# Optimization experiments

Hardware: AMD Instinct MI355X
Metric: run time of the kernel (lower is better)

The kernel has to match this reference:

```python
import jax, jax.numpy as jnp
import numpy as np


def _diag_perm(h, w):
    # Matches torch loop: offsets -(h-1)..w-1, within offset ordered by row i.
    ii, jj = np.meshgrid(np.arange(h), np.arange(w), indexing='ij')
    idx = np.lexsort((ii.ravel(), (jj - ii).ravel())).astype(np.int32)
    inv = np.argsort(idx).astype(np.int32)
    return jnp.asarray(idx), jnp.asarray(inv)


def _mamba(tok, ln_g, ln_b, Win, conv_w, conv_b, Wx, Wdt, bdt, A_log, Dp, Wout):
    # tok: (B, L, C). MambaLayer = LayerNorm + standard Mamba block.
    di, dc = conv_w.shape
    ds = A_log.shape[-1]
    dtr = Wdt.shape[-1]
    mu = tok.mean(-1, keepdims=True)
    var = ((tok - mu) ** 2).mean(-1, keepdims=True)
    t = (tok - mu) * jax.lax.rsqrt(var + 1e-5) * ln_g + ln_b
    xz = jnp.einsum('blc,ec->ble', t, Win)          # (B,L,2*di)
    xh, z = jnp.split(xz, 2, axis=-1)
    # causal depthwise conv over sequence
    xc = jnp.transpose(xh, (0, 2, 1))               # (B,di,L)
    xc = jax.lax.conv_general_dilated(
        xc, conv_w[:, None, :], (1,), [(dc - 1, 0)],
        dimension_numbers=('NCH', 'OIH', 'NCH'), feature_group_count=di)
    u = jax.nn.silu(jnp.transpose(xc, (0, 2, 1)) + conv_b)  # (B,L,di)
    proj = jnp.einsum('bld,ed->ble', u, Wx)
    dt_r, Bm, Cm = jnp.split(proj, [dtr, dtr + ds], axis=-1)
    dt = jax.nn.softplus(jnp.einsum('blr,dr->bld', dt_r, Wdt) + bdt)  # (B,L,di)
    A = -jnp.exp(A_log)                              # (di,ds)

    def step(h, inp):
        dt_t, B_t, C_t, u_t = inp                    # (B,di) (B,ds) (B,ds) (B,di)
        dA = jnp.exp(dt_t[..., None] * A)            # (B,di,ds)
        h = dA * h + dt_t[..., None] * B_t[:, None, :] * u_t[..., None]
        y = jnp.einsum('bds,bs->bd', h, C_t)
        return h, y

    h0 = jnp.zeros((u.shape[0], di, ds), u.dtype)
    _, ys = jax.lax.scan(step, h0, (jnp.moveaxis(dt, 1, 0), jnp.moveaxis(Bm, 1, 0),
                                    jnp.moveaxis(Cm, 1, 0), jnp.moveaxis(u, 1, 0)))
    y = jnp.moveaxis(ys, 0, 1) + u * Dp              # (B,L,di)
    y = y * jax.nn.silu(z)
    return jnp.einsum('bld,cd->blc', y, Wout)


def _forward(x, ln_g, ln_b, Win, conv_w, conv_b, Wx, Wdt, bdt, A_log, Dp, Wout):
    b, c, h, w = x.shape
    idx, inv = _diag_perm(h, w)

    def mam(d, tok):
        return _mamba(tok, ln_g[d], ln_b[d], Win[d], conv_w[d], conv_b[d],
                      Wx[d], Wdt[d], bdt[d], A_log[d], Dp[d], Wout[d])

    row_tok = x.reshape(b, c, h * w).transpose(0, 2, 1)
    row_feat = mam(0, row_tok).transpose(0, 2, 1).reshape(b, c, h, w)
    col_tok = x.transpose(0, 1, 3, 2).reshape(b, c, w * h).transpose(0, 2, 1)
    col_feat = mam(1, col_tok).transpose(0, 2, 1).reshape(b, c, w, h).transpose(0, 1, 3, 2)
    diag_feat = mam(2, row_tok[:, idx, :])[:, inv, :].transpose(0, 2, 1).reshape(b, c, h, w)
    xf = x[:, :, :, ::-1]
    anti_tok = xf.reshape(b, c, h * w).transpose(0, 2, 1)[:, idx, :]
    anti_feat = mam(3, anti_tok)[:, inv, :].transpose(0, 2, 1).reshape(b, c, h, w)[:, :, :, ::-1]
    gate = jax.nn.sigmoid((row_feat + col_feat + diag_feat + anti_feat) / 4.0)
    return x * gate


def setup_inputs() -> dict:
    key = jax.random.key(0)
    ks = jax.random.split(key, 8)
    B, C, H, W = 4, 96, 48, 48
    DI, DS, DC, DTR = 192, 16, 4, 6
    s = 0.05
    return {
        'x': jax.random.normal(ks[0], (B, C, H, W), jnp.float32),
        'ln_g': jnp.ones((4, C), jnp.float32),
        'ln_b': jnp.zeros((4, C), jnp.float32),
        'Win': jax.random.normal(ks[1], (4, 2 * DI, C), jnp.float32) * s,
        'conv_w': jax.random.normal(ks[2], (4, DI, DC), jnp.float32) * s,
        'conv_b': jnp.zeros((4, DI), jnp.float32),
        'Wx': jax.random.normal(ks[3], (4, DTR + 2 * DS, DI), jnp.float32) * s,
        'Wdt': jax.random.normal(ks[4], (4, DI, DTR), jnp.float32) * s,
        'bdt': jax.random.normal(ks[5], (4, DI), jnp.float32) * s,
        'A_log': jnp.log(jnp.broadcast_to(jnp.arange(1, DS + 1, dtype=jnp.float32), (4, DI, DS))),
        'Dp': jnp.ones((4, DI), jnp.float32),
        'Wout': jax.random.normal(ks[6], (4, C, DI), jnp.float32) * s,
    }


def reference(x, ln_g, ln_b, Win, conv_w, conv_b, Wx, Wdt, bdt, A_log, Dp, Wout):
    return _forward(x, ln_g, ln_b, Win, conv_w, conv_b, Wx, Wdt, bdt, A_log, Dp, Wout)
```

## Files before the change

### kernel.cpp

```cpp
#include <hip/hip_runtime.h>
#include <math.h>

#define LSEQ 2304
#define LC 32
#define NCH 72

typedef unsigned short u16;
typedef unsigned int u32;
typedef __attribute__((ext_vector_type(8))) short bf16x8;
typedef __attribute__((ext_vector_type(4))) float f32x4;

__device__ __forceinline__ float sigmoidf_(float v){ return 1.f/(1.f+__expf(-v)); }
__device__ __forceinline__ u16 f2b(float f){
  union{float f; u32 u;} v; v.f = f;
  u32 r = v.u + 0x7fffu + ((v.u >> 16) & 1u);
  return (u16)(r >> 16);
}
__device__ __forceinline__ float b2f(u16 h){
  union{u32 u; float f;} v; v.u = ((u32)h) << 16; return v.f;
}
__device__ __forceinline__ u16 f2h(float f){
  _Float16 h = (_Float16)f;
  union{_Float16 h; u16 u;} v; v.h = h; return v.u;
}
__device__ __forceinline__ float h2f(u16 u){
  union{u16 u; _Float16 h;} v; v.u = u; return (float)v.h;
}
__device__ __forceinline__ uint2 pack4(float a, float b, float c, float d){
  uint2 o;
  o.x = (u32)f2b(a) | ((u32)f2b(b) << 16);
  o.y = (u32)f2b(c) | ((u32)f2b(d) << 16);
  return o;
}
__device__ __forceinline__ float softplus_(float v){
  return fmaxf(v, 0.f) + __logf(1.f + __expf(-fabsf(v)));
}

__global__ void g_kernel(int* __restrict__ g, int* __restrict__ flag){
  int tid = threadIdx.x;
  if (tid == 0) *flag = 1;
  for (int l = tid; l < LSEQ; l += 256){
    g[l] = l;
    g[LSEQ + l] = (l % 48) * 48 + l / 48;
  }
  for (int p = tid; p < LSEQ; p += 256){
    int i = p / 48, j = p % 48, dd = j - i;
    int off = (dd <= 0) ? (47 + dd) * (48 + dd) / 2
                        : 1176 + 48 * (dd - 1) - dd * (dd - 1) / 2;
    int l = off + min(i, j);
    g[2 * LSEQ + l] = p;
  }
  __syncthreads();
  for (int l = tid; l < LSEQ; l += 256){
    int p2 = g[2 * LSEQ + l];
    g[3 * LSEQ + l] = (p2 / 48) * 48 + 47 - (p2 % 48);
  }
}

__global__ void prep_fold(const float* __restrict__ Win, const float* __restrict__ ln_g,
                          const float* __restrict__ ln_b, const float* __restrict__ A_log,
                          const float* __restrict__ Wout, const float* __restrict__ Wx,
                          const float* __restrict__ Wdt, const float* __restrict__ bdt,
                          u16* __restrict__ WinMF, float* __restrict__ b2,
                          float* __restrict__ Aneg2, u16* __restrict__ WoutMF,
                          u16* __restrict__ Wcomb, float* __restrict__ bcomb,
                          int* __restrict__ flag){
  int i = blockIdx.x * 256 + threadIdx.x;
  if (i < 4*192*16){
    float a = -expf(A_log[i]);
    Aneg2[i] = a * 1.44269504f;
    int s = i & 15;
    float a0 = -expf(A_log[i - s]);
    if (fabsf(a - (float)(s + 1) * a0) > 1e-5f * fabsf(a) + 1e-30f)
      atomicAnd(flag, 0);
  }
  if (i < 4*384*96){
    int d = i / 36864, r = i % 36864, c = r % 96;
    WinMF[i] = f2b(Win[i] * ln_g[d*96 + c]);
  }
  if (i < 4*96*192) WoutMF[i] = f2b(Wout[i]);
  if (i < 4*224*192){
    int d = i / 43008, r = i % 43008, e = r / 192, c = r % 192;
    float w;
    if (e < 192){
      const float* wdt = &Wdt[(size_t)(d*192 + e) * 6];
      w = 0.f;
      #pragma unroll
      for (int r6 = 0; r6 < 6; ++r6) w += wdt[r6] * Wx[(size_t)(d*38 + r6) * 192 + c];
    } else if (e < 208){
      w = Wx[(size_t)(d*38 + 6 + (e - 192)) * 192 + c];
    } else {
      w = Wx[(size_t)(d*38 + 22 + (e - 208)) * 192 + c];
    }
    Wcomb[i] = f2b(w);
  }
  if (i < 4*224){
    int d = i / 224, e = i % 224;
    bcomb[i] = (e < 192) ? bdt[d*192 + e] : 0.f;
  }
  if (i < 4*384){
    int d = i / 384;
    const float* wr = &Win[(size_t)i * 96];
    const float* lb = &ln_b[d * 96];
    float s = 0.f;
    for (int c = 0; c < 96; ++c) s += wr[c] * lb[c];
    b2[i] = s;
  }
}

__global__ __launch_bounds__(256) void ln_kernel(const float* __restrict__ x, u16* __restrict__ n){
  __shared__ float red[512];
  int tid = threadIdx.x;
  int s = tid & 63, q = tid >> 6;
  int T = blockIdx.x * 64 + s;
  int b = T / 2304, p = T % 2304;
  const float* xp = x + (size_t)b * 96 * 2304 + p;
  float vals[24];
  float sum = 0.f, ss = 0.f;
  #pragma unroll
  for (int k = 0; k < 24; ++k){
    float v = xp[(size_t)(q*24 + k) * 2304];
    vals[k] = v; sum += v; ss += v*v;
  }
  red[q*64 + s] = sum;
  red[256 + q*64 + s] = ss;
  __syncthreads();
  float S = red[s] + red[64+s] + red[128+s] + red[192+s];
  float Q = red[256+s] + red[320+s] + red[384+s] + red[448+s];
  float mu = S * (1.f/96.f);
  float var = Q * (1.f/96.f) - mu*mu;
  float rs = rsqrtf(var + 1e-5f);
  u32 w[12];
  #pragma unroll
  for (int k = 0; k < 12; ++k){
    float v0 = (vals[2*k]   - mu) * rs;
    float v1 = (vals[2*k+1] - mu) * rs;
    w[k] = (u32)f2b(v0) | ((u32)f2b(v1) << 16);
  }
  uint4* np_ = (uint4*)(n + (size_t)T * 96 + q*24);
  np_[0] = make_uint4(w[0], w[1], w[2],  w[3]);
  np_[1] = make_uint4(w[4], w[5], w[6],  w[7]);
  np_[2] = make_uint4(w[8], w[9], w[10], w[11]);
}

__global__ __launch_bounds__(256) void kproj(const u16* __restrict__ nbf,
    const u16* __restrict__ WinMF, const float* __restrict__ b2,
    u16* __restrict__ xz){
  int d = blockIdx.y;
  int wv = threadIdx.x >> 6, lane = threadIdx.x & 63;
  int lr = lane & 15, lg = lane >> 4;
  int r0 = blockIdx.x * 64 + wv * 16;
  const u16* Ap = nbf + (size_t)(r0 + lr) * 96 + lg * 8;
  bf16x8 tk0 = *(const bf16x8*)(Ap);
  bf16x8 tk1 = *(const bf16x8*)(Ap + 32);
  bf16x8 tk2 = *(const bf16x8*)(Ap + 64);
  const u16* Wb = WinMF + (size_t)d * 36864 + (size_t)lr * 96 + lg * 8;
  const float* b2d = b2 + d * 384;
  u16* out = xz + ((size_t)d * 9216 + r0 + lr) * 384;
  for (int grp = 0; grp < 3; ++grp){
    f32x4 acc[8];
    #pragma unroll
    for (int t = 0; t < 8; ++t)
      acc[t] = *(const f32x4*)&b2d[(grp*8 + t)*16 + lg*4];
    #pragma unroll
    for (int t = 0; t < 8; ++t){
      const u16* wp = Wb + (size_t)(grp*8 + t) * 1536;
      acc[t] = __builtin_amdgcn_mfma_f32_16x16x32_bf16(*(const bf16x8*)(wp     ), tk0, acc[t], 0, 0, 0);
      acc[t] = __builtin_amdgcn_mfma_f32_16x16x32_bf16(*(const bf16x8*)(wp + 32), tk1, acc[t], 0, 0, 0);
      acc[t] = __builtin_amdgcn_mfma_f32_16x16x32_bf16(*(const bf16x8*)(wp + 64), tk2, acc[t], 0, 0, 0);
    }
    #pragma unroll
    for (int t = 0; t < 8; ++t){
      uint2 o = pack4(acc[t][0], acc[t][1], acc[t][2], acc[t][3]);
      *(uint2*)&out[(grp*8 + t)*16 + lg*4] = o;
    }
  }
}

__global__ __launch_bounds__(256) void kconv(const u16* __restrict__ xz, const int* __restrict__ g,
    const float* __restrict__ conv_w, const float* __restrict__ conv_b,
    u16* __restrict__ u, u16* __restrict__ sz){
  __shared__ u16 xh[67][200];
  int d = blockIdx.z, b = blockIdx.y, l0 = blockIdx.x * 64;
  int tid = threadIdx.x;
  const int* gd = g + d * LSEQ;
  const u16* xzd = xz + (size_t)d * 9216 * 384 + (size_t)b * LSEQ * 384;
  for (int i = tid; i < 67*24; i += 256){
    int lt = i / 24, j = i % 24;
    int gl = l0 - 3 + lt;
    uint4 v = make_uint4(0u, 0u, 0u, 0u);
    if (gl >= 0){
      int p = gd[gl];
      v = *(const uint4*)(xzd + (size_t)p * 384 + j * 8);
    }
    *(uint4*)&xh[lt][j*8] = v;
  }
  size_t obase = ((size_t)(d*4 + b) * LSEQ + l0) * 192;
  for (int i = tid; i < 64*48; i += 256){
    int lt = i / 48, j = (i % 48) * 4;
    int p = gd[l0 + lt];
    uint2 zv = *(const uint2*)(xzd + (size_t)p * 384 + 192 + j);
    float z0 = b2f((u16)(zv.x & 0xffff)), z1 = b2f((u16)(zv.x >> 16));
    float z2 = b2f((u16)(zv.y & 0xffff)), z3 = b2f((u16)(zv.y >> 16));
    z0 *= sigmoidf_(z0); z1 *= sigmoidf_(z1); z2 *= sigmoidf_(z2); z3 *= sigmoidf_(z3);
    *(uint2*)(sz + obase + (size_t)lt * 192 + j) = pack4(z0, z1, z2, z3);
  }
  __syncthreads();
  for (int i = tid; i < 64*48; i += 256){
    int lt = i / 48, j = (i % 48) * 4;
    float a0 = conv_b[d*192 + j + 0];
    float a1 = conv_b[d*192 + j + 1];
    float a2 = conv_b[d*192 + j + 2];
    float a3 = conv_b[d*192 + j + 3];
    const float4 w0 = *(const float4*)&conv_w[(size_t)(d*192 + j + 0) * 4];
    const float4 w1 = *(const float4*)&conv_w[(size_t)(d*192 + j + 1) * 4];
    const float4 w2 = *(const float4*)&conv_w[(size_t)(d*192 + j + 2) * 4];
    const float4 w3 = *(const float4*)&conv_w[(size_t)(d*192 + j + 3) * 4];
    const float* w0p = (const float*)&w0;
    const float* w1p = (const float*)&w1;
    const float* w2p = (const float*)&w2;
    const float* w3p = (const float*)&w3;
    #pragma unroll
    for (int kk = 0; kk < 4; ++kk){
      uint2 xv = *(const uint2*)&xh[lt + kk][j];
      a0 += w0p[kk] * b2f((u16)(xv.x & 0xffff));
      a1 += w1p[kk] * b2f((u16)(xv.x >> 16));
      a2 += w2p[kk] * b2f((u16)(xv.y & 0xffff));
      a3 += w3p[kk] * b2f((u16)(xv.y >> 16));
    }
    a0 *= sigmoidf_(a0); a1 *= sigmoidf_(a1); a2 *= sigmoidf_(a2); a3 *= sigmoidf_(a3);
    *(uint2*)(u + obase + (size_t)lt * 192 + j) = pack4(a0, a1, a2, a3);
  }
}

__global__ __launch_bounds__(256) void kernBM(const u16* __restrict__ u,
    const u16* __restrict__ Wcomb, const float* __restrict__ bcomb,
    u16* __restrict__ dtb, float* __restrict__ Bm, float* __restrict__ Cm){
  __shared__ u16 ush[64 * 200];
  int d = blockIdx.y;
  int tid = threadIdx.x;
  int tile0 = blockIdx.x * 64;
  const u16* ub = u + ((size_t)d * 4 * LSEQ + tile0) * 192;
  for (int i = tid; i < 64*24; i += 256){
    int row = i / 24, c8 = i % 24;
    *(uint4*)&ush[row*200 + c8*8] = *(const uint4*)&ub[(size_t)row*192 + c8*8];
  }
  __syncthreads();
  int wv = tid >> 6, lane = tid & 63;
  int lr = lane & 15, lg = lane >> 4;
  const u16* urow = &ush[(wv*16 + lr)*200 + lg*8];
  bf16x8 tk[6];
  #pragma unroll
  for (int kc = 0; kc < 6; ++kc) tk[kc] = *(const bf16x8*)(urow + kc*32);
  const u16* Wb = Wcomb + (size_t)d * 224 * 192 + (size_t)lr * 192 + lg * 8;
  bf16x8 bw[2][6];
  #pragma unroll
  for (int kc = 0; kc < 6; ++kc) bw[0][kc] = *(const bf16x8*)(Wb + kc*32);
  size_t tokrow = (size_t)d * 4 * LSEQ + tile0 + wv*16 + lr;
  for (int t = 0; t < 14; ++t){
    int cur = t & 1;
    if (t < 13){
      const u16* wp = Wb + (size_t)(t + 1) * 3072;
      #pragma unroll
      for (int kc = 0; kc < 6; ++kc) bw[cur^1][kc] = *(const bf16x8*)(wp + kc*32);
    }
    f32x4 a = (f32x4){0.f, 0.f, 0.f, 0.f};
    #pragma unroll
    for (int kc = 0; kc < 6; ++kc)
      a = __builtin_amdgcn_mfma_f32_16x16x32_bf16(bw[cur][kc], tk[kc], a, 0, 0, 0);
    if (t < 12){
      f32x4 bb = *(const f32x4*)&bcomb[d*224 + t*16 + lg*4];
      float s0 = softplus_(a[0] + bb[0]);
      float s1 = softplus_(a[1] + bb[1]);
      float s2 = softplus_(a[2] + bb[2]);
      float s3 = softplus_(a[3] + bb[3]);
      uint2 o;
      o.x = (u32)f2h(s0) | ((u32)f2h(s1) << 16);
      o.y = (u32)f2h(s2) | ((u32)f2h(s3) << 16);
      *(uint2*)&dtb[tokrow * 192 + t*16 + lg*4] = o;
    } else if (t == 12){
      *(float4*)&Bm[tokrow * 16 + lg*4] = make_float4(a[0], a[1], a[2], a[3]);
    } else {
      *(float4*)&Cm[tokrow * 16 + lg*4] = make_float4(a[0], a[1], a[2], a[3]);
    }
  }
}

__global__ __launch_bounds__(192) void kernC1(const u16* __restrict__ dtb, const u16* __restrict__ u,
    const float* __restrict__ Bm, const float* __restrict__ Aneg2, const int* __restrict__ flag,
    u16* __restrict__ hfin, float* __restrict__ Send){
  __shared__ float Bsh[LC*16];
  int ch = blockIdx.x, b = blockIdx.y, d = blockIdx.z;
  int seq = d*4 + b;
  int di = threadIdx.x;
  size_t tb = (size_t)seq * LSEQ + ch * LC;
  const float* bp = Bm + tb * 16;
  for (int i = di; i < LC*16; i += 192) Bsh[i] = bp[i];
  const u16* dtp = dtb + tb * 192;
  const u16* up  = u   + tb * 192;
  float h[16];
  #pragma unroll
  for (int s = 0; s < 16; ++s) h[s] = 0.f;
  float Sacc = 0.f;
  __syncthreads();
  if (*flag){
    float A2_0 = Aneg2[(d*192 + di) * 16];
    for (int j = 0; j < LC; ++j){
      float dtv = h2f(dtp[j*192 + di]);
      float uv  = b2f(up[j*192 + di]);
      float Bs[16];
      {
        const float4* b4 = (const float4*)&Bsh[j * 16];
        #pragma unroll
        for (int q = 0; q < 4; ++q){ float4 v = b4[q]; Bs[q*4]=v.x; Bs[q*4+1]=v.y; Bs[q*4+2]=v.z; Bs[q*4+3]=v.w; }
      }
      float dtu = dtv * uv;
      float e1 = __builtin_amdgcn_exp2f(dtv * A2_0);
      float e2 = e1*e1, e4 = e2*e2, e8 = e4*e4;
      float p[8];
      p[0]=e1; p[1]=e2; p[2]=e1*e2; p[3]=e4; p[4]=e1*e4; p[5]=e2*e4; p[6]=p[2]*e4; p[7]=e8;
      #pragma unroll
      for (int s = 0; s < 8; ++s){
        h[s] = p[s]*h[s] + dtu*Bs[s];
        float q = p[s]*e8;
        h[s+8] = q*h[s+8] + dtu*Bs[s+8];
      }
      Sacc += dtv;
    }
  } else {
    float A2[16];
    {
      const float4* ap = (const float4*)&Aneg2[(d*192 + di) * 16];
      #pragma unroll
      for (int q = 0; q < 4; ++q){ float4 a4 = ap[q]; A2[q*4]=a4.x; A2[q*4+1]=a4.y; A2[q*4+2]=a4.z; A2[q*4+3]=a4.w; }
    }
    for (int j = 0; j < LC; ++j){
      float dtv = h2f(dtp[j*192 + di]);
      float uv  = b2f(up[j*192 + di]);
      float Bs[16];
      {
        const float4* b4 = (const float4*)&Bsh[j * 16];
        #pragma unroll
        for (int q = 0; q < 4; ++q){ float4 v = b4[q]; Bs[q*4]=v.x; Bs[q*4+1]=v.y; Bs[q*4+2]=v.z; Bs[q*4+3]=v.w; }
      }
      float dtu = dtv * uv;
      #pragma unroll
      for (int s = 0; s < 16; ++s)
        h[s] = __builtin_amdgcn_exp2f(dtv * A2[s]) * h[s] + dtu * Bs[s];
      Sacc += dtv;
    }
  }
  u16* hf = &hfin[((size_t)seq * NCH + ch) * 3072 + di * 16];
  uint4 o0, o1;
  o0.x = (u32)f2b(h[0])  | ((u32)f2b(h[1])  << 16);
  o0.y = (u32)f2b(h[2])  | ((u32)f2b(h[3])  << 16);
  o0.z = (u32)f2b(h[4])  | ((u32)f2b(h[5])  << 16);
  o0.w = (u32)f2b(h[6])  | ((u32)f2b(h[7])  << 16);
  o1.x = (u32)f2b(h[8])  | ((u32)f2b(h[9])  << 16);
  o1.y = (u32)f2b(h[10]) | ((u32)f2b(h[11]) << 16);
  o1.z = (u32)f2b(h[12]) | ((u32)f2b(h[13]) << 16);
  o1.w = (u32)f2b(h[14]) | ((u32)f2b(h[15]) << 16);
  *(uint4*)hf = o0;
  *(uint4*)(hf + 8) = o1;
  Send[((size_t)seq * NCH + ch) * 192 + di] = Sacc;
}

__global__ __launch_bounds__(256) void kernC2(const u16* __restrict__ hfin, const float* __restrict__ Send,
    const float* __restrict__ Aneg2, u16* __restrict__ hin){
  int t = blockIdx.x * 256 + threadIdx.x;
  int seq = t / 3072, q = t % 3072;
  int di = q >> 4, s = q & 15;
  int d = seq >> 2;
  float A2 = Aneg2[(d*192 + di)*16 + s];
  float hr = 0.f;
  const u16* hf = hfin + (size_t)seq * NCH * 3072 + q;
  u16* hi = hin + (size_t)seq * NCH * 3072 + q;
  const float* Se = Send + (size_t)seq * NCH * 192 + di;
  for (int ch = 0; ch < NCH; ++ch){
    hi[(size_t)ch * 3072] = f2b(hr);
    hr = b2f(hf[(size_t)ch * 3072]) + __builtin_amdgcn_exp2f(A2 * Se[(size_t)ch * 192]) * hr;
  }
}

__global__ __launch_bounds__(384) void kscan2out(const u16* __restrict__ dtb, const u16* __restrict__ u,
    const float* __restrict__ Bm, const float* __restrict__ Cm,
    const float* __restrict__ Aneg2, const int* __restrict__ flag, const u16* __restrict__ hin,
    const u16* __restrict__ sz, const float* __restrict__ Dp,
    const u16* __restrict__ WoutMF, const int* __restrict__ g,
    u16* __restrict__ feat){
  __shared__ float Bsh[64*16];
  __shared__ float Csh[64*16];
  __shared__ u16 vsh[64][200];
  int b = blockIdx.y, d = blockIdx.z;
  int seq = d*4 + b;
  int l0 = blockIdx.x * 64;
  int tid = threadIdx.x;
  int gc = tid / 192, di = tid % 192;
  int ch = blockIdx.x * 2 + gc;
  {
    const float* bp = Bm + ((size_t)seq * LSEQ + l0) * 16;
    const float* cp = Cm + ((size_t)seq * LSEQ + l0) * 16;
    for (int i = tid; i < 64*16; i += 384){ Bsh[i] = bp[i]; Csh[i] = cp[i]; }
  }
  float h[16];
  {
    const uint4* hi4 = (const uint4*)&hin[((size_t)seq * NCH + ch) * 3072 + di * 16];
    uint4 v0 = hi4[0], v1 = hi4[1];
    h[0]=b2f((u16)(v0.x&0xffff)); h[1]=b2f((u16)(v0.x>>16));
    h[2]=b2f((u16)(v0.y&0xffff)); h[3]=b2f((u16)(v0.y>>16));
    h[4]=b2f((u16)(v0.z&0xffff)); h[5]=b2f((u16)(v0.z>>16));
    h[6]=b2f((u16)(v0.w&0xffff)); h[7]=b2f((u16)(v0.w>>16));
    h[8]=b2f((u16)(v1.x&0xffff)); h[9]=b2f((u16)(v1.x>>16));
    h[10]=b2f((u16)(v1.y&0xffff)); h[11]=b2f((u16)(v1.y>>16));
    h[12]=b2f((u16)(v1.z&0xffff)); h[13]=b2f((u16)(v1.z>>16));
    h[14]=b2f((u16)(v1.w&0xffff)); h[15]=b2f((u16)(v1.w>>16));
  }
  float Dpv = Dp[d*192 + di];
  size_t tb = (size_t)seq * LSEQ + ch * LC;
  const u16* dtp = dtb + tb * 192;
  const u16* up  = u   + tb * 192;
  const u16* szp = sz  + tb * 192;
  __syncthreads();
  if (*flag){
    float A2_0 = Aneg2[(d*192 + di) * 16];
    for (int j = 0; j < LC; ++j){
      float dtv = h2f(dtp[j*192 + di]);
      float uv  = b2f(up[j*192 + di]);
      float Bs[16], Cs[16];
      {
        const float4* b4 = (const float4*)&Bsh[(gc*32 + j) * 16];
        const float4* c4 = (const float4*)&Csh[(gc*32 + j) * 16];
        #pragma unroll
        for (int q = 0; q < 4; ++q){
          float4 v = b4[q]; Bs[q*4]=v.x; Bs[q*4+1]=v.y; Bs[q*4+2]=v.z; Bs[q*4+3]=v.w;
          float4 w = c4[q]; Cs[q*4]=w.x; Cs[q*4+1]=w.y; Cs[q*4+2]=w.z; Cs[q*4+3]=w.w;
        }
      }
      float dtu = dtv * uv;
      float e1 = __builtin_amdgcn_exp2f(dtv * A2_0);
      float e2 = e1*e1, e4 = e2*e2, e8 = e4*e4;
      float p[8];
      p[0]=e1; p[1]=e2; p[2]=e1*e2; p[3]=e4; p[4]=e1*e4; p[5]=e2*e4; p[6]=p[2]*e4; p[7]=e8;
      float yv = 0.f;
      #pragma unroll
      for (int s = 0; s < 8; ++s){
        h[s] = p[s]*h[s] + dtu*Bs[s];
        yv += h[s]*Cs[s];
        float q = p[s]*e8;
        h[s+8] = q*h[s+8] + dtu*Bs[s+8];
        yv += h[s+8]*Cs[s+8];
      }
      float szv = b2f(szp[j*192 + di]);
      vsh[gc*32 + j][di] = f2b((yv + uv * Dpv) * szv);
    }
  } else {
    float A2[16];
    {
      const float4* ap = (const float4*)&Aneg2[(d*192 + di) * 16];
      #pragma unroll
      for (int q = 0; q < 4; ++q){ float4 a4 = ap[q]; A2[q*4]=a4.x; A2[q*4+1]=a4.y; A2[q*4+2]=a4.z; A2[q*4+3]=a4.w; }
    }
    for (int j = 0; j < LC; ++j){
      float dtv = h2f(dtp[j*192 + di]);
      float uv  = b2f(up[j*192 + di]);
      float Bs[16], Cs[16];
      {
        const float4* b4 = (const float4*)&Bsh[(gc*32 + j) * 16];
        const float4* c4 = (const float4*)&Csh[(gc*32 + j) * 16];
        #pragma unroll
        for (int q = 0; q < 4; ++q){
          float4 v = b4[q]; Bs[q*4]=v.x; Bs[q*4+1]=v.y; Bs[q*4+2]=v.z; Bs[q*4+3]=v.w;
          float4 w = c4[q]; Cs[q*4]=w.x; Cs[q*4+1]=w.y; Cs[q*4+2]=w.z; Cs[q*4+3]=w.w;
        }
      }
      float dtu = dtv * uv;
      float yv = 0.f;
      #pragma unroll
      for (int s = 0; s < 16; ++s){
        h[s] = __builtin_amdgcn_exp2f(dtv * A2[s]) * h[s] + dtu * Bs[s];
        yv += h[s] * Cs[s];
      }
      float szv = b2f(szp[j*192 + di]);
      vsh[gc*32 + j][di] = f2b((yv + uv * Dpv) * szv);
    }
  }
  __syncthreads();
  if (tid < 256){
    int wv = tid >> 6, lane = tid & 63;
    int lr = lane & 15, lg = lane >> 4;
    bf16x8 tk[6];
    #pragma unroll
    for (int kc = 0; kc < 6; ++kc)
      tk[kc] = *(const bf16x8*)&vsh[wv*16 + lr][kc*32 + lg*8];
    const u16* Wb = WoutMF + (size_t)d * 18432 + (size_t)lr * 192 + lg * 8;
    f32x4 acc[6];
    #pragma unroll
    for (int t = 0; t < 6; ++t) acc[t] = (f32x4){0.f, 0.f, 0.f, 0.f};
    #pragma unroll
    for (int t = 0; t < 6; ++t){
      const u16* wp = Wb + (size_t)t * 3072;
      #pragma unroll
      for (int kc = 0; kc < 6; ++kc)
        acc[t] = __builtin_amdgcn_mfma_f32_16x16x32_bf16(*(const bf16x8*)(wp + kc*32), tk[kc], acc[t], 0, 0, 0);
    }
    u16* fd = feat + (size_t)seq * LSEQ * 96;
    int p = g[d*LSEQ + l0 + wv*16 + lr];
    #pragma unroll
    for (int t = 0; t < 6; ++t){
      uint2 o = pack4(acc[t][0], acc[t][1], acc[t][2], acc[t][3]);
      *(uint2*)&fd[(size_t)p * 96 + t*16 + lg*4] = o;
    }
  }
}

__global__ __launch_bounds__(256) void kernE(const float* __restrict__ x, const u16* __restrict__ feat,
    float* __restrict__ out){
  __shared__ float acc[64 * 97];
  int p0 = blockIdx.x * 64, b = blockIdx.y;
  int tid = threadIdx.x;
  const size_t DS_ = (size_t)4 * LSEQ * 96;
  size_t base = ((size_t)b * LSEQ + p0) * 96;
  for (int i = tid; i < 3072; i += 256){
    int pp = i / 48, c2 = (i % 48) * 2;
    size_t o = base + (size_t)pp * 96 + c2;
    u32 v0 = *(const u32*)(feat + o);
    u32 v1 = *(const u32*)(feat + DS_ + o);
    u32 v2 = *(const u32*)(feat + 2*DS_ + o);
    u32 v3 = *(const u32*)(feat + 3*DS_ + o);
    float s0 = b2f((u16)(v0 & 0xffff)) + b2f((u16)(v1 & 0xffff)) + b2f((u16)(v2 & 0xffff)) + b2f((u16)(v3 & 0xffff));
    float s1 = b2f((u16)(v0 >> 16)) + b2f((u16)(v1 >> 16)) + b2f((u16)(v2 >> 16)) + b2f((u16)(v3 >> 16));
    acc[pp*97 + c2] = s0;
    acc[pp*97 + c2 + 1] = s1;
  }
  __syncthreads();
  for (int i = tid; i < 6144; i += 256){
    int c = i / 64, pp = i % 64;
    size_t o = ((size_t)b * 96 + c) * LSEQ + p0 + pp;
    out[o] = x[o] * sigmoidf_(acc[pp*97 + c] * 0.25f);
  }
}

extern "C" void kernel_launch(void* const* d_in, const int* in_sizes, int n_in,
                              void* d_out, int out_size, void* d_ws, size_t ws_size,
                              hipStream_t stream) {
  const float* x      = (const float*)d_in[0];
  const float* ln_g   = (const float*)d_in[1];
  const float* ln_b   = (const float*)d_in[2];
  const float* Win    = (const float*)d_in[3];
  const float* conv_w = (const float*)d_in[4];
  const float* conv_b = (const float*)d_in[5];
  const float* Wx     = (const float*)d_in[6];
  const float* Wdt    = (const float*)d_in[7];
  const float* bdt    = (const float*)d_in[8];
  const float* A_log  = (const float*)d_in[9];
  const float* Dp     = (const float*)d_in[10];
  const float* Wout   = (const float*)d_in[11];

  char* W = (char*)d_ws;
  char* W0 = W;
  auto alloc = [&](size_t bytes) -> char* {
    char* p = W; W += (bytes + 255) & ~(size_t)255; return p;
  };
  int*   g      = (int*)  alloc((size_t)4 * LSEQ * 4);
  int*   flag   = (int*)  alloc(256);
  float* Aneg2  = (float*)alloc((size_t)4 * 192 * 16 * 4);
  float* b2     = (float*)alloc((size_t)4 * 384 * 4);
  u16*   WinMF  = (u16*)  alloc((size_t)4 * 384 * 96 * 2);
  u16*   WoutMF = (u16*)  alloc((size_t)4 * 96 * 192 * 2);
  u16*   Wcomb  = (u16*)  alloc((size_t)4 * 224 * 192 * 2);
  float* bcomb  = (float*)alloc((size_t)4 * 224 * 4);
  u16*   nbf    = (u16*)  alloc((size_t)9216 * 96 * 2);
  u16*   xz     = (u16*)  alloc((size_t)4 * 9216 * 384 * 2);
  u16*   ubf    = (u16*)  alloc((size_t)16 * LSEQ * 192 * 2);
  u16*   szbf   = (u16*)  alloc((size_t)16 * LSEQ * 192 * 2);
  u16*   dtb    = (u16*)  alloc((size_t)16 * LSEQ * 192 * 2);
  float* Bm     = (float*)alloc((size_t)16 * LSEQ * 16 * 4);
  float* Cm     = (float*)alloc((size_t)16 * LSEQ * 16 * 4);
  float* Send   = (float*)alloc((size_t)16 * NCH * 192 * 4);
  u16*   hfin   = (u16*)  alloc((size_t)16 * NCH * 3072 * 2);
  u16*   hin    = (u16*)  alloc((size_t)16 * NCH * 3072 * 2);
  u16*   feat   = (u16*)  alloc((size_t)16 * LSEQ * 96 * 2);
  if ((size_t)(W - W0) > ws_size) return;

  g_kernel<<<1, 256, 0, stream>>>(g, flag);
  prep_fold<<<768, 256, 0, stream>>>(Win, ln_g, ln_b, A_log, Wout, Wx, Wdt, bdt,
                                     WinMF, b2, Aneg2, WoutMF, Wcomb, bcomb, flag);
  ln_kernel<<<144, 256, 0, stream>>>(x, nbf);
  kproj<<<dim3(144, 4), 256, 0, stream>>>(nbf, WinMF, b2, xz);
  kconv<<<dim3(36, 4, 4), 256, 0, stream>>>(xz, g, conv_w, conv_b, ubf, szbf);
  kernBM<<<dim3(144, 4), 256, 0, stream>>>(ubf, Wcomb, bcomb, dtb, Bm, Cm);
  kernC1<<<dim3(NCH, 4, 4), 192, 0, stream>>>(dtb, ubf, Bm, Aneg2, flag, hfin, Send);
  kernC2<<<192, 256, 0, stream>>>(hfin, Send, Aneg2, hin);
  kscan2out<<<dim3(36, 4, 4), 384, 0, stream>>>(dtb, ubf, Bm, Cm, Aneg2, flag, hin, szbf, Dp,
                                                WoutMF, g, feat);
  kernE<<<dim3(36, 4), 256, 0, stream>>>(x, feat, (float*)d_out);
}
```

Before: 197.0 us.

## Compute intra-chunk scan output in first pass and apply carried-state correction later

The first chunked scan pass now also computes the zero-initial-state output y and the cumulative dt sum per token, packed as two fp16 values, and writes them to a new buffer. The output pass no longer re-runs the recurrence. It adds a correction term exp(A*cumsum)·h_in·C to the stored y, which drops the B loads and the serial state update. In exchange it writes and reads an extra 4-byte-per-element buffer, and fp16 storage of y and the cumulative sum lowers precision.

```diff
diff --git a/kernel.cpp b/kernel.cpp
--- a/kernel.cpp
+++ b/kernel.cpp
@@ -287,17 +287,21 @@
 }
 
 __global__ __launch_bounds__(192) void kernC1(const u16* __restrict__ dtb, const u16* __restrict__ u,
-    const float* __restrict__ Bm, const float* __restrict__ Aneg2, const int* __restrict__ flag,
-    u16* __restrict__ hfin, float* __restrict__ Send){
+    const float* __restrict__ Bm, const float* __restrict__ Cm,
+    const float* __restrict__ Aneg2, const int* __restrict__ flag,
+    u16* __restrict__ hfin, float* __restrict__ Send, u32* __restrict__ yS){
   __shared__ float Bsh[LC*16];
+  __shared__ float Csh[LC*16];
   int ch = blockIdx.x, b = blockIdx.y, d = blockIdx.z;
   int seq = d*4 + b;
   int di = threadIdx.x;
   size_t tb = (size_t)seq * LSEQ + ch * LC;
   const float* bp = Bm + tb * 16;
-  for (int i = di; i < LC*16; i += 192) Bsh[i] = bp[i];
+  const float* cp = Cm + tb * 16;
+  for (int i = di; i < LC*16; i += 192){ Bsh[i] = bp[i]; Csh[i] = cp[i]; }
   const u16* dtp = dtb + tb * 192;
   const u16* up  = u   + tb * 192;
+  u32* ySp = yS + tb * 192;
   float h[16];
   #pragma unroll
   for (int s = 0; s < 16; ++s) h[s] = 0.f;
@@ -308,24 +312,32 @@
     for (int j = 0; j < LC; ++j){
       float dtv = h2f(dtp[j*192 + di]);
       float uv  = b2f(up[j*192 + di]);
-      float Bs[16];
+      float Bs[16], Cs[16];
       {
         const float4* b4 = (const float4*)&Bsh[j * 16];
+        const float4* c4 = (const float4*)&Csh[j * 16];
         #pragma unroll
-        for (int q = 0; q < 4; ++q){ float4 v = b4[q]; Bs[q*4]=v.x; Bs[q*4+1]=v.y; Bs[q*4+2]=v.z; Bs[q*4+3]=v.w; }
+        for (int q = 0; q < 4; ++q){
+          float4 v = b4[q]; Bs[q*4]=v.x; Bs[q*4+1]=v.y; Bs[q*4+2]=v.z; Bs[q*4+3]=v.w;
+          float4 w = c4[q]; Cs[q*4]=w.x; Cs[q*4+1]=w.y; Cs[q*4+2]=w.z; Cs[q*4+3]=w.w;
+        }
       }
       float dtu = dtv * uv;
       float e1 = __builtin_amdgcn_exp2f(dtv * A2_0);
       float e2 = e1*e1, e4 = e2*e2, e8 = e4*e4;
       float p[8];
       p[0]=e1; p[1]=e2; p[2]=e1*e2; p[3]=e4; p[4]=e1*e4; p[5]=e2*e4; p[6]=p[2]*e4; p[7]=e8;
+      float yv = 0.f;
       #pragma unroll
       for (int s = 0; s < 8; ++s){
         h[s] = p[s]*h[s] + dtu*Bs[s];
+        yv += h[s]*Cs[s];
         float q = p[s]*e8;
         h[s+8] = q*h[s+8] + dtu*Bs[s+8];
+        yv += h[s+8]*Cs[s+8];
       }
       Sacc += dtv;
+      ySp[j*192 + di] = (u32)f2h(yv) | ((u32)f2h(Sacc) << 16);
     }
   } else {
     float A2[16];
@@ -337,17 +349,25 @@
     for (int j = 0; j < LC; ++j){
       float dtv = h2f(dtp[j*192 + di]);
       float uv  = b2f(up[j*192 + di]);
-      float Bs[16];
+      float Bs[16], Cs[16];
       {
         const float4* b4 = (const float4*)&Bsh[j * 16];
+        const float4* c4 = (const float4*)&Csh[j * 16];
         #pragma unroll
-        for (int q = 0; q < 4; ++q){ float4 v = b4[q]; Bs[q*4]=v.x; Bs[q*4+1]=v.y; Bs[q*4+2]=v.z; Bs[q*4+3]=v.w; }
+        for (int q = 0; q < 4; ++q){
+          float4 v = b4[q]; Bs[q*4]=v.x; Bs[q*4+1]=v.y; Bs[q*4+2]=v.z; Bs[q*4+3]=v.w;
+          float4 w = c4[q]; Cs[q*4]=w.x; Cs[q*4+1]=w.y; Cs[q*4+2]=w.z; Cs[q*4+3]=w.w;
+        }
       }
       float dtu = dtv * uv;
-      #pragma unroll
-      for (int s = 0; s < 16; ++s)
+      float yv = 0.f;
+      #pragma unroll
+      for (int s = 0; s < 16; ++s){
         h[s] = __builtin_amdgcn_exp2f(dtv * A2[s]) * h[s] + dtu * Bs[s];
+        yv += h[s] * Cs[s];
+      }
       Sacc += dtv;
+      ySp[j*192 + di] = (u32)f2h(yv) | ((u32)f2h(Sacc) << 16);
     }
   }
   u16* hf = &hfin[((size_t)seq * NCH + ch) * 3072 + di * 16];
@@ -382,13 +402,12 @@
   }
 }
 
-__global__ __launch_bounds__(384) void kscan2out(const u16* __restrict__ dtb, const u16* __restrict__ u,
-    const float* __restrict__ Bm, const float* __restrict__ Cm,
+__global__ __launch_bounds__(384) void kscan2out(const u32* __restrict__ yS, const u16* __restrict__ u,
+    const float* __restrict__ Cm,
     const float* __restrict__ Aneg2, const int* __restrict__ flag, const u16* __restrict__ hin,
     const u16* __restrict__ sz, const float* __restrict__ Dp,
     const u16* __restrict__ WoutMF, const int* __restrict__ g,
     u16* __restrict__ feat){
-  __shared__ float Bsh[64*16];
   __shared__ float Csh[64*16];
   __shared__ u16 vsh[64][200];
   int b = blockIdx.y, d = blockIdx.z;
@@ -398,60 +417,53 @@
   int gc = tid / 192, di = tid % 192;
   int ch = blockIdx.x * 2 + gc;
   {
-    const float* bp = Bm + ((size_t)seq * LSEQ + l0) * 16;
     const float* cp = Cm + ((size_t)seq * LSEQ + l0) * 16;
-    for (int i = tid; i < 64*16; i += 384){ Bsh[i] = bp[i]; Csh[i] = cp[i]; }
-  }
-  float h[16];
+    for (int i = tid; i < 64*16; i += 384) Csh[i] = cp[i];
+  }
+  float hs[16];
   {
     const uint4* hi4 = (const uint4*)&hin[((size_t)seq * NCH + ch) * 3072 + di * 16];
     uint4 v0 = hi4[0], v1 = hi4[1];
-    h[0]=b2f((u16)(v0.x&0xffff)); h[1]=b2f((u16)(v0.x>>16));
-    h[2]=b2f((u16)(v0.y&0xffff)); h[3]=b2f((u16)(v0.y>>16));
-    h[4]=b2f((u16)(v0.z&0xffff)); h[5]=b2f((u16)(v0.z>>16));
-    h[6]=b2f((u16)(v0.w&0xffff)); h[7]=b2f((u16)(v0.w>>16));
-    h[8]=b2f((u16)(v1.x&0xffff)); h[9]=b2f((u16)(v1.x>>16));
-    h[10]=b2f((u16)(v1.y&0xffff)); h[11]=b2f((u16)(v1.y>>16));
-    h[12]=b2f((u16)(v1.z&0xffff)); h[13]=b2f((u16)(v1.z>>16));
-    h[14]=b2f((u16)(v1.w&0xffff)); h[15]=b2f((u16)(v1.w>>16));
+    hs[0]=b2f((u16)(v0.x&0xffff)); hs[1]=b2f((u16)(v0.x>>16));
+    hs[2]=b2f((u16)(v0.y&0xffff)); hs[3]=b2f((u16)(v0.y>>16));
+    hs[4]=b2f((u16)(v0.z&0xffff)); hs[5]=b2f((u16)(v0.z>>16));
+    hs[6]=b2f((u16)(v0.w&0xffff)); hs[7]=b2f((u16)(v0.w>>16));
+    hs[8]=b2f((u16)(v1.x&0xffff)); hs[9]=b2f((u16)(v1.x>>16));
+    hs[10]=b2f((u16)(v1.y&0xffff)); hs[11]=b2f((u16)(v1.y>>16));
+    hs[12]=b2f((u16)(v1.z&0xffff)); hs[13]=b2f((u16)(v1.z>>16));
+    hs[14]=b2f((u16)(v1.w&0xffff)); hs[15]=b2f((u16)(v1.w>>16));
   }
   float Dpv = Dp[d*192 + di];
   size_t tb = (size_t)seq * LSEQ + ch * LC;
-  const u16* dtp = dtb + tb * 192;
+  const u32* ySp = yS + tb * 192;
   const u16* up  = u   + tb * 192;
   const u16* szp = sz  + tb * 192;
   __syncthreads();
   if (*flag){
     float A2_0 = Aneg2[(d*192 + di) * 16];
     for (int j = 0; j < LC; ++j){
-      float dtv = h2f(dtp[j*192 + di]);
+      u32 ys = ySp[j*192 + di];
+      float yv = h2f((u16)(ys & 0xffff));
+      float Sc = h2f((u16)(ys >> 16));
       float uv  = b2f(up[j*192 + di]);
-      float Bs[16], Cs[16];
+      float Cs[16];
       {
-        const float4* b4 = (const float4*)&Bsh[(gc*32 + j) * 16];
         const float4* c4 = (const float4*)&Csh[(gc*32 + j) * 16];
         #pragma unroll
-        for (int q = 0; q < 4; ++q){
-          float4 v = b4[q]; Bs[q*4]=v.x; Bs[q*4+1]=v.y; Bs[q*4+2]=v.z; Bs[q*4+3]=v.w;
-          float4 w = c4[q]; Cs[q*4]=w.x; Cs[q*4+1]=w.y; Cs[q*4+2]=w.z; Cs[q*4+3]=w.w;
-        }
+        for (int q = 0; q < 4; ++q){ float4 w = c4[q]; Cs[q*4]=w.x; Cs[q*4+1]=w.y; Cs[q*4+2]=w.z; Cs[q*4+3]=w.w; }
       }
-      float dtu = dtv * uv;
-      float e1 = __builtin_amdgcn_exp2f(dtv * A2_0);
+      float e1 = __builtin_amdgcn_exp2f(Sc * A2_0);
       float e2 = e1*e1, e4 = e2*e2, e8 = e4*e4;
       float p[8];
       p[0]=e1; p[1]=e2; p[2]=e1*e2; p[3]=e4; p[4]=e1*e4; p[5]=e2*e4; p[6]=p[2]*e4; p[7]=e8;
-      float yv = 0.f;
+      float corr = 0.f;
       #pragma unroll
       for (int s = 0; s < 8; ++s){
-        h[s] = p[s]*h[s] + dtu*Bs[s];
-        yv += h[s]*Cs[s];
-        float q = p[s]*e8;
-        h[s+8] = q*h[s+8] + dtu*Bs[s+8];
-        yv += h[s+8]*Cs[s+8];
+        corr += p[s]     * hs[s]   * Cs[s];
+        corr += p[s]*e8  * hs[s+8] * Cs[s+8];
       }
       float szv = b2f(szp[j*192 + di]);
-      vsh[gc*32 + j][di] = f2b((yv + uv * Dpv) * szv);
+      vsh[gc*32 + j][di] = f2b((yv + corr + uv * Dpv) * szv);
     }
   } else {
     float A2[16];
@@ -461,27 +473,22 @@
       for (int q = 0; q < 4; ++q){ float4 a4 = ap[q]; A2[q*4]=a4.x; A2[q*4+1]=a4.y; A2[q*4+2]=a4.z; A2[q*4+3]=a4.w; }
     }
     for (int j = 0; j < LC; ++j){
-      float dtv = h2f(dtp[j*192 + di]);
+      u32 ys = ySp[j*192 + di];
+      float yv = h2f((u16)(ys & 0xffff));
+      float Sc = h2f((u16)(ys >> 16));
       float uv  = b2f(up[j*192 + di]);
-      float Bs[16], Cs[16];
+      float Cs[16];
       {
-        const float4* b4 = (const float4*)&Bsh[(gc*32 + j) * 16];
         const float4* c4 = (const float4*)&Csh[(gc*32 + j) * 16];
         #pragma unroll
-        for (int q = 0; q < 4; ++q){
-          float4 v = b4[q]; Bs[q*4]=v.x; Bs[q*4+1]=v.y; Bs[q*4+2]=v.z; Bs[q*4+3]=v.w;
-          float4 w = c4[q]; Cs[q*4]=w.x; Cs[q*4+1]=w.y; Cs[q*4+2]=w.z; Cs[q*4+3]=w.w;
-        }
+        for (int q = 0; q < 4; ++q){ float4 w = c4[q]; Cs[q*4]=w.x; Cs[q*4+1]=w.y; Cs[q*4+2]=w.z; Cs[q*4+3]=w.w; }
       }
-      float dtu = dtv * uv;
-      float yv = 0.f;
-      #pragma unroll
-      for (int s = 0; s < 16; ++s){
-        h[s] = __builtin_amdgcn_exp2f(dtv * A2[s]) * h[s] + dtu * Bs[s];
-        yv += h[s] * Cs[s];
-      }
+      float corr = 0.f;
+      #pragma unroll
+      for (int s = 0; s < 16; ++s)
+        corr += __builtin_amdgcn_exp2f(Sc * A2[s]) * hs[s] * Cs[s];
       float szv = b2f(szp[j*192 + di]);
-      vsh[gc*32 + j][di] = f2b((yv + uv * Dpv) * szv);
+      vsh[gc*32 + j][di] = f2b((yv + corr + uv * Dpv) * szv);
     }
   }
   __syncthreads();
@@ -576,6 +583,7 @@
   u16*   dtb    = (u16*)  alloc((size_t)16 * LSEQ * 192 * 2);
   float* Bm     = (float*)alloc((size_t)16 * LSEQ * 16 * 4);
   float* Cm     = (float*)alloc((size_t)16 * LSEQ * 16 * 4);
+  u32*   ySbuf  = (u32*)  alloc((size_t)16 * LSEQ * 192 * 4);
   float* Send   = (float*)alloc((size_t)16 * NCH * 192 * 4);
   u16*   hfin   = (u16*)  alloc((size_t)16 * NCH * 3072 * 2);
   u16*   hin    = (u16*)  alloc((size_t)16 * NCH * 3072 * 2);
@@ -589,9 +597,9 @@
   kproj<<<dim3(144, 4), 256, 0, stream>>>(nbf, WinMF, b2, xz);
   kconv<<<dim3(36, 4, 4), 256, 0, stream>>>(xz, g, conv_w, conv_b, ubf, szbf);
   kernBM<<<dim3(144, 4), 256, 0, stream>>>(ubf, Wcomb, bcomb, dtb, Bm, Cm);
-  kernC1<<<dim3(NCH, 4, 4), 192, 0, stream>>>(dtb, ubf, Bm, Aneg2, flag, hfin, Send);
+  kernC1<<<dim3(NCH, 4, 4), 192, 0, stream>>>(dtb, ubf, Bm, Cm, Aneg2, flag, hfin, Send, ySbuf);
   kernC2<<<192, 256, 0, stream>>>(hfin, Send, Aneg2, hin);
-  kscan2out<<<dim3(36, 4, 4), 384, 0, stream>>>(dtb, ubf, Bm, Cm, Aneg2, flag, hin, szbf, Dp,
+  kscan2out<<<dim3(36, 4, 4), 384, 0, stream>>>(ySbuf, ubf, Cm, Aneg2, flag, hin, szbf, Dp,
                                                 WoutMF, g, feat);
   kernE<<<dim3(36, 4), 256, 0, stream>>>(x, feat, (float*)d_out);
 }
```

Result: no change. 199.1 us (+1.1%).
